# Kernel optimization log

Measured on AMD Instinct MI355X. Metric: run time of the kernel, lower is better.

The kernel has to match this reference:

```python
import jax, jax.numpy as jnp
import numpy as np

EPS = 1e-5

def _layernorm(x, w, b):
    mu = jnp.mean(x, axis=-1, keepdims=True)
    var = jnp.mean(jnp.square(x - mu), axis=-1, keepdims=True)
    return (x - mu) * jax.lax.rsqrt(var + EPS) * w + b

def setup_inputs() -> dict:
    key = jax.random.key(0)
    ks = jax.random.split(key, 8)
    L, D, FF = 4096, 768, 3072
    s = 1.0 / np.sqrt(D)
    return {
        "x": jax.random.normal(ks[0], (L, D), jnp.float32),
        "in_proj_w": jax.random.normal(ks[1], (3 * D, D), jnp.float32) * s,
        "in_proj_b": jnp.zeros((3 * D,), jnp.float32),
        "out_w": jax.random.normal(ks[2], (D, D), jnp.float32) * s,
        "out_b": jnp.zeros((D,), jnp.float32),
        "ln1_w": jnp.ones((D,), jnp.float32),
        "ln1_b": jnp.zeros((D,), jnp.float32),
        "ln2_w": jnp.ones((D,), jnp.float32),
        "ln2_b": jnp.zeros((D,), jnp.float32),
        "ff_w1": jax.random.normal(ks[3], (FF, D), jnp.float32) * s,
        "ff_b1": jnp.zeros((FF,), jnp.float32),
        "ff_w2": jax.random.normal(ks[4], (D, FF), jnp.float32) * (1.0 / np.sqrt(FF)),
        "ff_b2": jnp.zeros((D,), jnp.float32),
        "window": 128,
    }

def reference(x, in_proj_w, in_proj_b, out_w, out_b, ln1_w, ln1_b, ln2_w, ln2_b, ff_w1, ff_b1, ff_w2, ff_b2, window):
    L, D = x.shape
    H = 12
    hd = D // H
    # packed qkv projection (torch MultiheadAttention in_proj)
    qkv = x @ in_proj_w.T + in_proj_b          # [L, 3D]
    q, k, v = jnp.split(qkv, 3, axis=-1)
    q = q.reshape(L, H, hd).transpose(1, 0, 2)  # [H, L, hd]
    k = k.reshape(L, H, hd).transpose(1, 0, 2)
    v = v.reshape(L, H, hd).transpose(1, 0, 2)
    scores = jnp.einsum('hqd,hkd->hqk', q, k) / np.sqrt(hd)  # [H, L, L]
    idx = jnp.arange(L)
    banned = jnp.abs(idx[:, None] - idx[None, :]) > window    # True = disallowed
    scores = jnp.where(banned[None], -jnp.inf, scores)
    probs = jax.nn.softmax(scores, axis=-1)
    ctx = jnp.einsum('hqk,hkd->hqd', probs, v)               # [H, L, hd]
    ctx = ctx.transpose(1, 0, 2).reshape(L, D)
    attn_out = ctx @ out_w.T + out_b
    h = _layernorm(x + attn_out, ln1_w, ln1_b)
    ff = jax.nn.gelu(h @ ff_w1.T + ff_b1, approximate=False) @ ff_w2.T + ff_b2
    return _layernorm(h + ff, ln2_w, ln2_b)
```

## Files before the change

### kernel.cpp

```cpp
#include <hip/hip_runtime.h>

typedef __bf16 bf16x8 __attribute__((ext_vector_type(8)));
typedef float f32x4 __attribute__((ext_vector_type(4)));

__device__ __forceinline__ unsigned short f2b(float f) {
    unsigned int u = __float_as_uint(f);
    u = (u + 0x7fffu + ((u >> 16) & 1u)) >> 16;
    return (unsigned short)u;
}

__global__ __launch_bounds__(256) void cvt_f2b(const float* __restrict__ s,
                                               unsigned short* __restrict__ d, int n4) {
    int i = blockIdx.x * 256 + threadIdx.x;
    if (i < n4) {
        float4 v = ((const float4*)s)[i];
        ushort4 o;
        o.x = f2b(v.x); o.y = f2b(v.y); o.z = f2b(v.z); o.w = f2b(v.w);
        ((ushort4*)d)[i] = o;
    }
}

#define GL16(g, s) __builtin_amdgcn_global_load_lds( \
    (const __attribute__((address_space(1))) unsigned int*)(g), \
    (__attribute__((address_space(3))) unsigned int*)(s), 16, 0, 0)

template<int EPI>
__global__ __launch_bounds__(256) void gemm_nt(
    const unsigned short* __restrict__ A,
    const unsigned short* __restrict__ B,
    const float* __restrict__ bias,
    float* __restrict__ Cf, unsigned short* __restrict__ Cb,
    int M, int N, int K)
{
    __shared__ __align__(16) unsigned short As[128 * 64];
    __shared__ __align__(16) unsigned short Bs[128 * 64];
    const int tid = threadIdx.x;
    const int l = tid & 63;
    const int w = tid >> 6;
    const int wr = w >> 1, wc = w & 1;
    const long arow = (long)blockIdx.y * 128 + (tid >> 3);
    const long brow = (long)blockIdx.x * 128 + (tid >> 3);
    const int kc = (tid & 7) * 8;
    const unsigned short* Ap = A + arow * K + kc;
    const unsigned short* Bp = B + brow * K + kc;

    f32x4 acc[4][4] = {};

    for (int k0 = 0; k0 < K; k0 += 64) {
#pragma unroll
        for (int i = 0; i < 4; ++i) {
            GL16(Ap + k0 + (long)32 * i * K, As + i * 2048 + tid * 8);
            GL16(Bp + k0 + (long)32 * i * K, Bs + i * 2048 + tid * 8);
        }
        __syncthreads();
#pragma unroll
        for (int kk = 0; kk < 2; ++kk) {
            bf16x8 a[4], b[4];
#pragma unroll
            for (int m = 0; m < 4; ++m)
                a[m] = *(const bf16x8*)&As[(wr * 64 + m * 16 + (l & 15)) * 64 + kk * 32 + (l >> 4) * 8];
#pragma unroll
            for (int n = 0; n < 4; ++n)
                b[n] = *(const bf16x8*)&Bs[(wc * 64 + n * 16 + (l & 15)) * 64 + kk * 32 + (l >> 4) * 8];
#pragma unroll
            for (int m = 0; m < 4; ++m)
#pragma unroll
                for (int n = 0; n < 4; ++n)
                    acc[m][n] = __builtin_amdgcn_mfma_f32_16x16x32_bf16(a[m], b[n], acc[m][n], 0, 0, 0);
        }
        __syncthreads();
    }

    const int r0 = blockIdx.y * 128 + wr * 64 + ((l >> 4) << 2);
    const int c0 = blockIdx.x * 128 + wc * 64 + (l & 15);
#pragma unroll
    for (int n = 0; n < 4; ++n) {
        const int col = c0 + n * 16;
        const float bv = bias[col];
#pragma unroll
        for (int m = 0; m < 4; ++m) {
#pragma unroll
            for (int r = 0; r < 4; ++r) {
                long row = r0 + m * 16 + r;
                float v = acc[m][n][r] + bv;
                if (EPI == 2) v = 0.5f * v * (1.0f + erff(v * 0.70710678f));
                if (EPI == 1) Cf[row * N + col] = v;
                else          Cb[row * N + col] = f2b(v);
            }
        }
    }
}

__global__ __launch_bounds__(256) void attn_local(
    const unsigned short* __restrict__ qkv,
    unsigned short* __restrict__ ctx,
    const int* __restrict__ winp)
{
    const int L = 4096;
    const int W = *winp;
    const int h = blockIdx.y;
    const int q0 = blockIdx.x * 64;
    const int tid = threadIdx.x;
    const int w = tid >> 6, l = tid & 63;
    __shared__ __align__(16) unsigned short Qs[64 * 64];
    __shared__ __align__(16) unsigned short Ks[64 * 64];
    __shared__ __align__(16) unsigned short Vs[64 * 64];
    __shared__ __align__(16) unsigned short Ps[64 * 64];

    {
        const int cg = tid & 7;
#pragma unroll
        for (int i = 0; i < 2; ++i) {
            int r = (tid >> 3) + 32 * i;
            uint4 v = *(const uint4*)&qkv[(long)(q0 + r) * 2304 + h * 64 + cg * 8];
            *(uint4*)&Qs[r * 64 + ((cg ^ (r & 7)) << 3)] = v;
        }
    }

    float mrow[4], lrow[4];
    f32x4 o[4] = {};
#pragma unroll
    for (int r = 0; r < 4; ++r) { mrow[r] = -1e30f; lrow[r] = 0.0f; }

    for (int st = 0; st < 5; ++st) {
        const int k0 = q0 - 128 + st * 64;
        __syncthreads();
        {
            const int cg = tid & 7;
#pragma unroll
            for (int i = 0; i < 2; ++i) {
                int r = (tid >> 3) + 32 * i;
                int kr = k0 + r;
                int krc = kr < 0 ? 0 : (kr >= L ? L - 1 : kr);
                uint4 kv = *(const uint4*)&qkv[(long)krc * 2304 + 768 + h * 64 + cg * 8];
                *(uint4*)&Ks[r * 64 + ((cg ^ (r & 7)) << 3)] = kv;
                uint4 vv = *(const uint4*)&qkv[(long)krc * 2304 + 1536 + h * 64 + cg * 8];
#pragma unroll
                for (int jj = 0; jj < 4; ++jj) {
                    unsigned int word = (jj == 0) ? vv.x : (jj == 1) ? vv.y : (jj == 2) ? vv.z : vv.w;
                    int d0 = cg * 8 + jj * 2;
                    int d1 = d0 + 1;
                    Vs[d0 * 64 + (((r >> 3) ^ (d0 & 7)) << 3) + (r & 7)] = (unsigned short)(word & 0xffffu);
                    Vs[d1 * 64 + (((r >> 3) ^ (d1 & 7)) << 3) + (r & 7)] = (unsigned short)(word >> 16);
                }
            }
        }
        __syncthreads();

        f32x4 s[4] = {};
#pragma unroll
        for (int kk = 0; kk < 2; ++kk) {
            const int aro = w * 16 + (l & 15);
            bf16x8 aq = *(const bf16x8*)&Qs[aro * 64 + (((kk * 4 + (l >> 4)) ^ (aro & 7)) << 3)];
#pragma unroll
            for (int n = 0; n < 4; ++n) {
                const int bro = n * 16 + (l & 15);
                bf16x8 bk = *(const bf16x8*)&Ks[bro * 64 + (((kk * 4 + (l >> 4)) ^ (bro & 7)) << 3)];
                s[n] = __builtin_amdgcn_mfma_f32_16x16x32_bf16(aq, bk, s[n], 0, 0, 0);
            }
        }

        const int qrow = q0 + w * 16 + ((l >> 4) << 2);
        const int kcol = k0 + (l & 15);
        float p[4][4];
#pragma unroll
        for (int n = 0; n < 4; ++n) {
#pragma unroll
            for (int r = 0; r < 4; ++r) {
                int key = kcol + n * 16;
                int q = qrow + r;
                int dd = q - key; if (dd < 0) dd = -dd;
                bool banned = (key < 0) || (key >= L) || (dd > W);
                p[n][r] = banned ? -1e30f : s[n][r] * 0.125f;
            }
        }
        float mx[4];
#pragma unroll
        for (int r = 0; r < 4; ++r)
            mx[r] = fmaxf(fmaxf(p[0][r], p[1][r]), fmaxf(p[2][r], p[3][r]));
#pragma unroll
        for (int off = 8; off >= 1; off >>= 1)
#pragma unroll
            for (int r = 0; r < 4; ++r)
                mx[r] = fmaxf(mx[r], __shfl_xor(mx[r], off));

        float sc[4], mn[4];
#pragma unroll
        for (int r = 0; r < 4; ++r) {
            mn[r] = fmaxf(mrow[r], mx[r]);
            sc[r] = __expf(mrow[r] - mn[r]);
            mrow[r] = mn[r];
        }
        float rs[4] = {0.f, 0.f, 0.f, 0.f};
#pragma unroll
        for (int n = 0; n < 4; ++n)
#pragma unroll
            for (int r = 0; r < 4; ++r) {
                float pv = __expf(p[n][r] - mn[r]);
                p[n][r] = pv;
                rs[r] += pv;
            }
#pragma unroll
        for (int off = 8; off >= 1; off >>= 1)
#pragma unroll
            for (int r = 0; r < 4; ++r)
                rs[r] += __shfl_xor(rs[r], off);
#pragma unroll
        for (int r = 0; r < 4; ++r)
            lrow[r] = lrow[r] * sc[r] + rs[r];
#pragma unroll
        for (int n = 0; n < 4; ++n)
#pragma unroll
            for (int r = 0; r < 4; ++r)
                o[n][r] *= sc[r];

#pragma unroll
        for (int n = 0; n < 4; ++n) {
            int col = n * 16 + (l & 15);
            int cb = col >> 3, ci = col & 7;
#pragma unroll
            for (int r = 0; r < 4; ++r) {
                int rp = w * 16 + ((l >> 4) << 2) + r;
                Ps[rp * 64 + ((cb ^ (rp & 7)) << 3) + ci] = f2b(p[n][r]);
            }
        }
#pragma unroll
        for (int kk = 0; kk < 2; ++kk) {
            const int aro = w * 16 + (l & 15);
            bf16x8 ap = *(const bf16x8*)&Ps[aro * 64 + (((kk * 4 + (l >> 4)) ^ (aro & 7)) << 3)];
#pragma unroll
            for (int n = 0; n < 4; ++n) {
                const int bro = n * 16 + (l & 15);
                bf16x8 bv = *(const bf16x8*)&Vs[bro * 64 + (((kk * 4 + (l >> 4)) ^ (bro & 7)) << 3)];
                o[n] = __builtin_amdgcn_mfma_f32_16x16x32_bf16(ap, bv, o[n], 0, 0, 0);
            }
        }
    }

#pragma unroll
    for (int n = 0; n < 4; ++n) {
        int col = h * 64 + n * 16 + (l & 15);
#pragma unroll
        for (int r = 0; r < 4; ++r) {
            int q = q0 + w * 16 + ((l >> 4) << 2) + r;
            ctx[(long)q * 768 + col] = f2b(o[n][r] / lrow[r]);
        }
    }
}

__global__ __launch_bounds__(256) void ln_res(
    const float* __restrict__ Ain, const float* __restrict__ Bin,
    const float* __restrict__ w, const float* __restrict__ bb,
    float* __restrict__ outf, unsigned short* __restrict__ outb)
{
    const int D = 768;
    const int row = blockIdx.x;
    const int t = threadIdx.x;
    const float* pa = Ain + (long)row * D;
    const float* pb = Bin + (long)row * D;
    float x0 = pa[t] + pb[t];
    float x1 = pa[t + 256] + pb[t + 256];
    float x2 = pa[t + 512] + pb[t + 512];
    float s = x0 + x1 + x2;
    float ss = x0 * x0 + x1 * x1 + x2 * x2;
#pragma unroll
    for (int off = 32; off >= 1; off >>= 1) {
        s += __shfl_xor(s, off);
        ss += __shfl_xor(ss, off);
    }
    __shared__ float sm[8];
    if ((t & 63) == 0) { sm[t >> 6] = s; sm[(t >> 6) + 4] = ss; }
    __syncthreads();
    s = sm[0] + sm[1] + sm[2] + sm[3];
    ss = sm[4] + sm[5] + sm[6] + sm[7];
    float mu = s * (1.0f / 768.0f);
    float var = ss * (1.0f / 768.0f) - mu * mu;
    float rstd = rsqrtf(var + 1e-5f);
    float* po = outf + (long)row * D;
#pragma unroll
    for (int i = 0; i < 3; ++i) {
        int c = t + i * 256;
        float x = (i == 0) ? x0 : (i == 1) ? x1 : x2;
        float y = (x - mu) * rstd * w[c] + bb[c];
        po[c] = y;
        if (outb) outb[(long)row * D + c] = f2b(y);
    }
}

extern "C" void kernel_launch(void* const* d_in, const int* in_sizes, int n_in,
                              void* d_out, int out_size, void* d_ws, size_t ws_size,
                              hipStream_t stream) {
    const float* x   = (const float*)d_in[0];
    const float* ipw = (const float*)d_in[1];
    const float* ipb = (const float*)d_in[2];
    const float* ow  = (const float*)d_in[3];
    const float* ob  = (const float*)d_in[4];
    const float* l1w = (const float*)d_in[5];
    const float* l1b = (const float*)d_in[6];
    const float* l2w = (const float*)d_in[7];
    const float* l2b = (const float*)d_in[8];
    const float* fw1 = (const float*)d_in[9];
    const float* fb1 = (const float*)d_in[10];
    const float* fw2 = (const float*)d_in[11];
    const float* fb2 = (const float*)d_in[12];
    const int*   win = (const int*)d_in[13];

    const int L = 4096, D = 768, TD = 2304, FF = 3072;
    char* p = (char*)d_ws;
    unsigned short* xb   = (unsigned short*)p; p += (size_t)L * D * 2;
    unsigned short* wqkv = (unsigned short*)p; p += (size_t)TD * D * 2;
    unsigned short* wout = (unsigned short*)p; p += (size_t)D * D * 2;
    unsigned short* wf1  = (unsigned short*)p; p += (size_t)FF * D * 2;
    unsigned short* wf2  = (unsigned short*)p; p += (size_t)FF * D * 2;
    unsigned short* ctxb = (unsigned short*)p; p += (size_t)L * D * 2;
    float* tmpf          = (float*)p;          p += (size_t)L * D * 4;
    float* hf            = (float*)p;          p += (size_t)L * D * 4;
    unsigned short* big  = (unsigned short*)p; p += (size_t)L * FF * 2;
    unsigned short* qkvb = big;
    unsigned short* gb   = big;
    unsigned short* hb   = ctxb;

    cvt_f2b<<<(L * D / 4 + 255) / 256, 256, 0, stream>>>(x, xb, L * D / 4);
    cvt_f2b<<<(TD * D / 4 + 255) / 256, 256, 0, stream>>>(ipw, wqkv, TD * D / 4);
    cvt_f2b<<<(D * D / 4 + 255) / 256, 256, 0, stream>>>(ow, wout, D * D / 4);
    cvt_f2b<<<(FF * D / 4 + 255) / 256, 256, 0, stream>>>(fw1, wf1, FF * D / 4);
    cvt_f2b<<<(FF * D / 4 + 255) / 256, 256, 0, stream>>>(fw2, wf2, FF * D / 4);

    gemm_nt<0><<<dim3(TD / 128, L / 128), 256, 0, stream>>>(xb, wqkv, ipb, nullptr, qkvb, L, TD, D);
    attn_local<<<dim3(L / 64, 12), 256, 0, stream>>>(qkvb, ctxb, win);
    gemm_nt<1><<<dim3(D / 128, L / 128), 256, 0, stream>>>(ctxb, wout, ob, tmpf, nullptr, L, D, D);
    ln_res<<<L, 256, 0, stream>>>(x, tmpf, l1w, l1b, hf, hb);
    gemm_nt<2><<<dim3(FF / 128, L / 128), 256, 0, stream>>>(hb, wf1, fb1, nullptr, gb, L, FF, D);
    gemm_nt<1><<<dim3(D / 128, L / 128), 256, 0, stream>>>(gb, wf2, fb2, tmpf, nullptr, L, D, FF);
    ln_res<<<L, 256, 0, stream>>>(hf, tmpf, l2w, l2b, (float*)d_out, nullptr);
}
```

Baseline: 340.6 us.

## Split-K with atomics for narrow GEMMs, XCD block swizzle, merge conversion launches

Merges the five fp32-to-bf16 conversion kernels into one launch with hardcoded range offsets. Adds a block-index swizzle to the GEMM that spreads consecutive workgroups across eight groups, apparently to match the chiplet layout. Runs the two N=768 GEMMs (out-proj and FF2) as 4-way split-K with atomic fp32 adds into a pre-zeroed buffer, so the small 192-block grids fill more CUs. The trade is an extra zeroing pass and atomic traffic, and the float summation order is no longer fixed.

```diff
diff --git a/kernel.cpp b/kernel.cpp
--- a/kernel.cpp
+++ b/kernel.cpp
@@ -9,15 +9,29 @@
     return (unsigned short)u;
 }
 
-__global__ __launch_bounds__(256) void cvt_f2b(const float* __restrict__ s,
-                                               unsigned short* __restrict__ d, int n4) {
+__global__ __launch_bounds__(256) void cvt_all(
+    const float* __restrict__ s0, unsigned short* __restrict__ d0,
+    const float* __restrict__ s1, unsigned short* __restrict__ d1,
+    const float* __restrict__ s2, unsigned short* __restrict__ d2,
+    const float* __restrict__ s3, unsigned short* __restrict__ d3,
+    const float* __restrict__ s4, unsigned short* __restrict__ d4)
+{
     int i = blockIdx.x * 256 + threadIdx.x;
-    if (i < n4) {
-        float4 v = ((const float4*)s)[i];
-        ushort4 o;
-        o.x = f2b(v.x); o.y = f2b(v.y); o.z = f2b(v.z); o.w = f2b(v.w);
-        ((ushort4*)d)[i] = o;
-    }
+    const float* s; unsigned short* d; int j;
+    if (i < 786432)       { s = s0; d = d0; j = i; }
+    else if (i < 1228800) { s = s1; d = d1; j = i - 786432; }
+    else if (i < 1376256) { s = s2; d = d2; j = i - 1228800; }
+    else if (i < 1966080) { s = s3; d = d3; j = i - 1376256; }
+    else                  { s = s4; d = d4; j = i - 1966080; }
+    float4 v = ((const float4*)s)[j];
+    ushort4 o;
+    o.x = f2b(v.x); o.y = f2b(v.y); o.z = f2b(v.z); o.w = f2b(v.w);
+    ((ushort4*)d)[j] = o;
+}
+
+__global__ __launch_bounds__(256) void zero_f32(float4* __restrict__ p, int n4) {
+    int i = blockIdx.x * 256 + threadIdx.x;
+    if (i < n4) p[i] = make_float4(0.f, 0.f, 0.f, 0.f);
 }
 
 #define GL16(g, s) __builtin_amdgcn_global_load_lds( \
@@ -34,19 +48,30 @@
 {
     __shared__ __align__(16) unsigned short As[128 * 64];
     __shared__ __align__(16) unsigned short Bs[128 * 64];
+    const int nwg = gridDim.x * gridDim.y;
+    const int lin = blockIdx.y * gridDim.x + blockIdx.x;
+    const int qq = nwg >> 3;
+    const int swz = (lin & 7) * qq + (lin >> 3);
+    const int bx = swz % gridDim.x;
+    const int by = swz / gridDim.x;
+
     const int tid = threadIdx.x;
     const int l = tid & 63;
     const int w = tid >> 6;
     const int wr = w >> 1, wc = w & 1;
-    const long arow = (long)blockIdx.y * 128 + (tid >> 3);
-    const long brow = (long)blockIdx.x * 128 + (tid >> 3);
+    const long arow = (long)by * 128 + (tid >> 3);
+    const long brow = (long)bx * 128 + (tid >> 3);
     const int kc = (tid & 7) * 8;
     const unsigned short* Ap = A + arow * K + kc;
     const unsigned short* Bp = B + brow * K + kc;
 
+    const int kslice = K / gridDim.z;
+    const int kbeg = blockIdx.z * kslice;
+    const int kend = kbeg + kslice;
+
     f32x4 acc[4][4] = {};
 
-    for (int k0 = 0; k0 < K; k0 += 64) {
+    for (int k0 = kbeg; k0 < kend; k0 += 64) {
 #pragma unroll
         for (int i = 0; i < 4; ++i) {
             GL16(Ap + k0 + (long)32 * i * K, As + i * 2048 + tid * 8);
@@ -71,8 +96,8 @@
         __syncthreads();
     }
 
-    const int r0 = blockIdx.y * 128 + wr * 64 + ((l >> 4) << 2);
-    const int c0 = blockIdx.x * 128 + wc * 64 + (l & 15);
+    const int r0 = by * 128 + wr * 64 + ((l >> 4) << 2);
+    const int c0 = bx * 128 + wc * 64 + (l & 15);
 #pragma unroll
     for (int n = 0; n < 4; ++n) {
         const int col = c0 + n * 16;
@@ -82,10 +107,16 @@
 #pragma unroll
             for (int r = 0; r < 4; ++r) {
                 long row = r0 + m * 16 + r;
-                float v = acc[m][n][r] + bv;
-                if (EPI == 2) v = 0.5f * v * (1.0f + erff(v * 0.70710678f));
-                if (EPI == 1) Cf[row * N + col] = v;
-                else          Cb[row * N + col] = f2b(v);
+                float v = acc[m][n][r];
+                if (EPI == 3) {
+                    if (blockIdx.z == 0) v += bv;
+                    unsafeAtomicAdd(&Cf[row * N + col], v);
+                } else {
+                    v += bv;
+                    if (EPI == 2) v = 0.5f * v * (1.0f + erff(v * 0.70710678f));
+                    if (EPI == 1) Cf[row * N + col] = v;
+                    else          Cb[row * N + col] = f2b(v);
+                }
             }
         }
     }
@@ -320,17 +351,15 @@
     unsigned short* gb   = big;
     unsigned short* hb   = ctxb;
 
-    cvt_f2b<<<(L * D / 4 + 255) / 256, 256, 0, stream>>>(x, xb, L * D / 4);
-    cvt_f2b<<<(TD * D / 4 + 255) / 256, 256, 0, stream>>>(ipw, wqkv, TD * D / 4);
-    cvt_f2b<<<(D * D / 4 + 255) / 256, 256, 0, stream>>>(ow, wout, D * D / 4);
-    cvt_f2b<<<(FF * D / 4 + 255) / 256, 256, 0, stream>>>(fw1, wf1, FF * D / 4);
-    cvt_f2b<<<(FF * D / 4 + 255) / 256, 256, 0, stream>>>(fw2, wf2, FF * D / 4);
-
-    gemm_nt<0><<<dim3(TD / 128, L / 128), 256, 0, stream>>>(xb, wqkv, ipb, nullptr, qkvb, L, TD, D);
+    cvt_all<<<9984, 256, 0, stream>>>(x, xb, ipw, wqkv, ow, wout, fw1, wf1, fw2, wf2);
+
+    gemm_nt<0><<<dim3(TD / 128, L / 128, 1), 256, 0, stream>>>(xb, wqkv, ipb, nullptr, qkvb, L, TD, D);
     attn_local<<<dim3(L / 64, 12), 256, 0, stream>>>(qkvb, ctxb, win);
-    gemm_nt<1><<<dim3(D / 128, L / 128), 256, 0, stream>>>(ctxb, wout, ob, tmpf, nullptr, L, D, D);
+    zero_f32<<<(L * D / 4 + 255) / 256, 256, 0, stream>>>((float4*)tmpf, L * D / 4);
+    gemm_nt<3><<<dim3(D / 128, L / 128, 4), 256, 0, stream>>>(ctxb, wout, ob, tmpf, nullptr, L, D, D);
     ln_res<<<L, 256, 0, stream>>>(x, tmpf, l1w, l1b, hf, hb);
-    gemm_nt<2><<<dim3(FF / 128, L / 128), 256, 0, stream>>>(hb, wf1, fb1, nullptr, gb, L, FF, D);
-    gemm_nt<1><<<dim3(D / 128, L / 128), 256, 0, stream>>>(gb, wf2, fb2, tmpf, nullptr, L, D, FF);
+    gemm_nt<2><<<dim3(FF / 128, L / 128, 1), 256, 0, stream>>>(hb, wf1, fb1, nullptr, gb, L, FF, D);
+    zero_f32<<<(L * D / 4 + 255) / 256, 256, 0, stream>>>((float4*)tmpf, L * D / 4);
+    gemm_nt<3><<<dim3(D / 128, L / 128, 4), 256, 0, stream>>>(gb, wf2, fb2, tmpf, nullptr, L, D, FF);
     ln_res<<<L, 256, 0, stream>>>(hf, tmpf, l2w, l2b, (float*)d_out, nullptr);
 }
```

Result: slower. 368.7 us (+8.2%).
